# Performance work log

Measured on AMD Instinct MI355X. Metric: run time of the kernel, lower is better.

The kernel has to match this reference:

```python
import jax, jax.numpy as jnp
import numpy as np

B, S, HID, NH = 2, 2048, 1024, 16
HD = HID // NH  # head_dim = 64


def setup_inputs() -> dict:
    key = jax.random.key(0)
    ks = jax.random.split(key, 9)
    init = 0.02
    return {
        "x": jax.random.normal(ks[0], (B, S, HID), dtype=jnp.float32),
        "Wq": jax.random.normal(ks[1], (HID, HID), dtype=jnp.float32) * init,
        "bq": jnp.zeros((HID,), dtype=jnp.float32),
        "Wk": jax.random.normal(ks[2], (HID, HID), dtype=jnp.float32) * init,
        "bk": jnp.zeros((HID,), dtype=jnp.float32),
        "Wv": jax.random.normal(ks[3], (HID, HID), dtype=jnp.float32) * init,
        "bv": jnp.zeros((HID,), dtype=jnp.float32),
        "Wo": jax.random.normal(ks[4], (HID, HID), dtype=jnp.float32) * init,
        "bo": jnp.zeros((HID,), dtype=jnp.float32),
    }


def _split_heads(t):
    # [B, S, HID] -> [B, NH, S, HD]
    return t.reshape(B, S, NH, HD).transpose(0, 2, 1, 3)


def reference(x, Wq, bq, Wk, bk, Wv, bv, Wo, bo):
    q = _split_heads(x @ Wq.T + bq)
    k = _split_heads(x @ Wk.T + bk)
    v = _split_heads(x @ Wv.T + bv)

    # Faithful to source: scores = QK^T / (head_dim ** -0.5) == QK^T * sqrt(head_dim)
    inv_scale = jnp.asarray(HD ** (-0.5), dtype=x.dtype)
    scores = jnp.einsum("bhqd,bhkd->bhqk", q, k) / inv_scale

    causal_mask = jnp.triu(jnp.ones((S, S), dtype=bool), k=1)  # True above diagonal
    scores = jnp.where(causal_mask, jnp.asarray(-jnp.inf, dtype=scores.dtype), scores)
    attn = jax.nn.softmax(scores, axis=-1)  # dropout = identity (eval mode)

    ctx = jnp.einsum("bhqk,bhkd->bhqd", attn, v)
    ctx = ctx.transpose(0, 2, 1, 3).reshape(B, S, HID)
    out = ctx @ Wo.T + bo  # out_layer Linear; dropout = identity
    return out, attn
```

## Files before the change

### kernel.cpp

```cpp
#include <hip/hip_runtime.h>
#include <hip/hip_bf16.h>

#define BB   2
#define SS   2048
#define HID  1024
#define NH   16
#define HD   64
#define NEGS -30000.0f

typedef __bf16 bf16x8 __attribute__((ext_vector_type(8)));
typedef __bf16 bf16x4 __attribute__((ext_vector_type(4)));
typedef float  f32x4  __attribute__((ext_vector_type(4)));

static __device__ __forceinline__ f32x4 mfma_bf16(bf16x8 a, bf16x8 b, f32x4 c) {
    return __builtin_amdgcn_mfma_f32_16x16x32_bf16(a, b, c, 0, 0, 0);
}

static __device__ __forceinline__ void split_bf16(float f, __bf16* hp, __bf16* lp) {
    __bf16 h = (__bf16)f;
    *hp = h;
    *lp = (__bf16)(f - (float)h);
}

static __device__ __forceinline__ float clampf(float v, float lo, float hi) {
    return fminf(fmaxf(v, lo), hi);
}

static __device__ __forceinline__ void gll16(const __bf16* g, __bf16* l) {
    __builtin_amdgcn_global_load_lds((const void*)g, (void*)l, 16, 0, 0);
}

static __device__ __forceinline__ void barrier_lds() {
    asm volatile("s_waitcnt lgkmcnt(0)" ::: "memory");
    __builtin_amdgcn_sched_barrier(0);
    __builtin_amdgcn_s_barrier();
    __builtin_amdgcn_sched_barrier(0);
}

__global__ __launch_bounds__(256) void split_kernel(
    const float* __restrict__ x,
    const float* __restrict__ Wq, const float* __restrict__ Wk,
    const float* __restrict__ Wv, const float* __restrict__ Wo,
    __bf16* __restrict__ xh, __bf16* __restrict__ xl,
    __bf16* __restrict__ wqh, __bf16* __restrict__ wql,
    __bf16* __restrict__ wkh, __bf16* __restrict__ wkl,
    __bf16* __restrict__ wvh, __bf16* __restrict__ woh)
{
    const int which = blockIdx.y;
    const int i4 = blockIdx.x * 256 + threadIdx.x;
    if (which == 0) {
        const float4 v = ((const float4*)x)[i4];
        const float* p = (const float*)&v;
        bf16x4 h4, l4v;
#pragma unroll
        for (int j = 0; j < 4; j++) { __bf16 hh, ll; split_bf16(p[j], &hh, &ll); h4[j] = hh; l4v[j] = ll; }
        *(bf16x4*)&xh[(size_t)i4 * 4] = h4;
        *(bf16x4*)&xl[(size_t)i4 * 4] = l4v;
        return;
    }
    if (i4 >= (HID * HID) / 4) return;
    const float* src = which == 1 ? Wq : which == 2 ? Wk : which == 3 ? Wv : Wo;
    const float sc = (which == 1) ? 8.0f : 1.0f;
    const float4 v = ((const float4*)src)[i4];
    const float* p = (const float*)&v;
    bf16x4 h4, l4v;
#pragma unroll
    for (int j = 0; j < 4; j++) { __bf16 hh, ll; split_bf16(p[j] * sc, &hh, &ll); h4[j] = hh; l4v[j] = ll; }
    if (which == 1)      { *(bf16x4*)&wqh[(size_t)i4 * 4] = h4; *(bf16x4*)&wql[(size_t)i4 * 4] = l4v; }
    else if (which == 2) { *(bf16x4*)&wkh[(size_t)i4 * 4] = h4; *(bf16x4*)&wkl[(size_t)i4 * 4] = l4v; }
    else if (which == 3) { *(bf16x4*)&wvh[(size_t)i4 * 4] = h4; }
    else                 { *(bf16x4*)&woh[(size_t)i4 * 4] = h4; }
}

__global__ __launch_bounds__(256) void qkv_kernel(
    const __bf16* __restrict__ xh, const __bf16* __restrict__ xl,
    const __bf16* __restrict__ wqh, const __bf16* __restrict__ wql,
    const __bf16* __restrict__ wkh, const __bf16* __restrict__ wkl,
    const __bf16* __restrict__ wvh,
    const float* __restrict__ bq, const float* __restrict__ bk, const float* __restrict__ bv,
    __bf16* __restrict__ qh, __bf16* __restrict__ ql,
    __bf16* __restrict__ kh, __bf16* __restrict__ kl,
    __bf16* __restrict__ vt)
{
    __shared__ __align__(16) __bf16 smem[18432];
    __bf16* const Ah = smem;
    __bf16* const Al = smem + 4096;
    __bf16* const Bh = smem + 8192;
    __bf16* const Bl = smem + 12288;

    const int stream = blockIdx.x >> 3, ct = blockIdx.x & 7;
    const int t0 = blockIdx.y * 128, c0 = ct * 128;
    const bool qk = stream < 2;
    const __bf16* const Bhg = stream == 0 ? wqh : stream == 1 ? wkh : wvh;
    const __bf16* const Blg = stream == 0 ? wql : wkl;
    const float* const bias = stream == 0 ? bq : stream == 1 ? bk : bv;
    const float bscale = stream == 0 ? 8.0f : 1.0f;

    const int tid = threadIdx.x, wave = tid >> 6, lane = tid & 63;
    const int l16 = lane & 15, quad = lane >> 4;
    const int wr = wave >> 1, wc = wave & 1;

    const int ar0 = tid >> 2,         as0 = (tid & 3) ^ (ar0 & 3);
    const int ar1 = (256 + tid) >> 2, as1 = ((256 + tid) & 3) ^ (ar1 & 3);
    const size_t aoff0 = (size_t)(t0 + ar0) * HID + as0 * 8;
    const size_t aoff1 = (size_t)(t0 + ar1) * HID + as1 * 8;
    const size_t boff0 = (size_t)(c0 + ar0) * HID + as0 * 8;
    const size_t boff1 = (size_t)(c0 + ar1) * HID + as1 * 8;
    const int ld0 = wave << 9, ld1 = (4 + wave) << 9;

    const f32x4 zero4 = {0.f, 0.f, 0.f, 0.f};
    f32x4 acc[4][4];
#pragma unroll
    for (int i = 0; i < 4; i++)
#pragma unroll
        for (int j = 0; j < 4; j++) acc[i][j] = zero4;

    for (int k0 = 0; k0 < HID; k0 += 32) {
        __syncthreads();
        gll16(xh + aoff0 + k0, Ah + ld0);
        gll16(xh + aoff1 + k0, Ah + ld1);
        gll16(Bhg + boff0 + k0, Bh + ld0);
        gll16(Bhg + boff1 + k0, Bh + ld1);
        if (qk) {
            gll16(xl + aoff0 + k0, Al + ld0);
            gll16(xl + aoff1 + k0, Al + ld1);
            gll16(Blg + boff0 + k0, Bl + ld0);
            gll16(Blg + boff1 + k0, Bl + ld1);
        }
        __syncthreads();

        bf16x8 aH[4], aL[4], bHf[4], bLf[4];
#pragma unroll
        for (int mf = 0; mf < 4; mf++) {
            const int row = wr * 64 + mf * 16 + l16;
            const int off = row * 32 + ((quad ^ (row & 3)) << 3);
            aH[mf] = *(const bf16x8*)(Ah + off);
            if (qk) aL[mf] = *(const bf16x8*)(Al + off);
        }
#pragma unroll
        for (int nf = 0; nf < 4; nf++) {
            const int row = wc * 64 + nf * 16 + l16;
            const int off = row * 32 + ((quad ^ (row & 3)) << 3);
            bHf[nf] = *(const bf16x8*)(Bh + off);
            if (qk) bLf[nf] = *(const bf16x8*)(Bl + off);
        }
#pragma unroll
        for (int mf = 0; mf < 4; mf++)
#pragma unroll
            for (int nf = 0; nf < 4; nf++) {
                acc[mf][nf] = mfma_bf16(aH[mf], bHf[nf], acc[mf][nf]);
                if (qk) {
                    acc[mf][nf] = mfma_bf16(aH[mf], bLf[nf], acc[mf][nf]);
                    acc[mf][nf] = mfma_bf16(aL[mf], bHf[nf], acc[mf][nf]);
                }
            }
    }

    const int bidx = t0 >> 11;
    const int s0 = t0 & (SS - 1);

    if (qk) {
        __bf16* const Es = smem;
        __bf16* const hi_arr = stream == 0 ? qh : kh;
        __bf16* const lo_arr = stream == 0 ? ql : kl;
#pragma unroll
        for (int pass = 0; pass < 2; pass++) {
            __syncthreads();
#pragma unroll
            for (int nf = 0; nf < 4; nf++) {
                const int dcl = wc * 64 + nf * 16 + l16;
                const float bv_ = bias[c0 + dcl] * bscale;
#pragma unroll
                for (int mf = 0; mf < 4; mf++)
#pragma unroll
                    for (int r = 0; r < 4; r++) {
                        const int srl = wr * 64 + mf * 16 + quad * 4 + r;
                        const float v = clampf(acc[mf][nf][r] + bv_, -1e4f, 1e4f);
                        __bf16 hv, lv;
                        split_bf16(v, &hv, &lv);
                        Es[srl * 132 + dcl] = pass ? lv : hv;
                    }
            }
            __syncthreads();
            __bf16* const dst = pass ? lo_arr : hi_arr;
#pragma unroll
            for (int i = 0; i < 8; i++) {
                const int idx = tid + i * 256;
                const int row = idx >> 4, c16 = idx & 15;
                const int hh = (c0 >> 6) + (c16 >> 3);
                const int dd = (c16 & 7) * 8;
                const size_t o = ((size_t)(bidx * NH + hh) * SS + (s0 + row)) * HD + dd;
                *(uint4*)&dst[o] = *(const uint4*)&Es[row * 132 + c16 * 8];
            }
        }
    } else {
        __syncthreads();
        __bf16* const Vts = smem + wave * 4608;
#pragma unroll
        for (int nf = 0; nf < 4; nf++) {
            const int dloc = nf * 16 + l16;
            const float bv_ = bias[c0 + wc * 64 + dloc];
#pragma unroll
            for (int mf = 0; mf < 4; mf++)
#pragma unroll
                for (int r = 0; r < 4; r++)
                    Vts[dloc * 72 + mf * 16 + quad * 4 + r] =
                        (__bf16)clampf(acc[mf][nf][r] + bv_, -1e4f, 1e4f);
        }
        const int hh = (c0 + wc * 64) >> 6;
        const size_t vb = (size_t)(bidx * NH + hh) * HD * SS;
        const int sc0 = s0 + wr * 64;
#pragma unroll
        for (int j = 0; j < 8; j++) {
            const int idx = j * 64 + lane;
            const int d = idx >> 3, c8 = idx & 7;
            *(uint4*)&vt[vb + (size_t)d * SS + sc0 + c8 * 8] =
                *(const uint4*)&Vts[d * 72 + c8 * 8];
        }
    }
}

__global__ __launch_bounds__(512) void attn_kernel(
    const __bf16* __restrict__ qh, const __bf16* __restrict__ ql,
    const __bf16* __restrict__ kh, const __bf16* __restrict__ kl,
    const __bf16* __restrict__ vt,
    float* __restrict__ attn, __bf16* __restrict__ ctx)
{
    __shared__ __align__(16) __bf16 Kh0[4096], Kl0[4096], Kh1[4096], Kl1[4096];
    __shared__ __align__(16) __bf16 Vt0[4096], Vt1[4096];
    __shared__ __align__(16) __bf16 Ps[128][72];
    __shared__ __align__(16) __bf16 _occ_pad[8192];

    const int bid = blockIdx.x;
    const int g   = bid & 7;
    const int ii  = bid >> 3;
    const int bh  = g + 8 * (ii & 3);
    const int p   = ii >> 2;
    const int b   = bh >> 4, h = bh & 15;

    const int tid  = threadIdx.x;
    const int wave = tid >> 6, lane = tid & 63;
    const int l16  = lane & 15, quad = lane >> 4;

    const int sr = tid >> 3, ssw = (tid & 7) ^ (sr & 7);
    const size_t kq = (size_t)sr * HD + ssw * 8;
    const size_t vq = (size_t)sr * SS + ssw * 8;
    const int ldw = wave << 9;

    const __bf16* const khp = kh + (size_t)bh * SS * HD;
    const __bf16* const klp = kl + (size_t)bh * SS * HD;
    const __bf16* const vtp = vt + (size_t)bh * HD * SS;

#define STAGE_K(j_, KH, KL) do {                                  \
        const __bf16* kg_ = khp + (size_t)(j_) * (64 * HD);       \
        const __bf16* lg_ = klp + (size_t)(j_) * (64 * HD);       \
        gll16(kg_ + kq, (KH) + ldw); gll16(lg_ + kq, (KL) + ldw); \
    } while (0)
#define STAGE_V(j_, VT) do {                                      \
        const __bf16* vg_ = vtp + (size_t)(j_) * 64;              \
        gll16(vg_ + vq, (VT) + ldw);                              \
    } while (0)

    const f32x4 zero4 = {0.f, 0.f, 0.f, 0.f};

    for (int seg = 0; seg < 2; seg++) {
        const int qt = seg ? p : (15 - p);
        const int nj = 2 * qt + 2;

        bf16x8 aHq[2], aLq[2];
        {
            const size_t qrow = ((size_t)bh * SS + qt * 128 + wave * 16 + l16) * HD;
#pragma unroll
            for (int ks = 0; ks < 2; ks++) {
                aHq[ks] = *(const bf16x8*)&qh[qrow + ks * 32 + quad * 8];
                aLq[ks] = *(const bf16x8*)&ql[qrow + ks * 32 + quad * 8];
            }
        }

        float m4[4], l4[4];
#pragma unroll
        for (int r = 0; r < 4; r++) { m4[r] = NEGS; l4[r] = 0.f; }

        __syncthreads();
        STAGE_K(0, Kh0, Kl0);
        __syncthreads();

        for (int j = 0; j < nj; j++) {
            if (j) __syncthreads();
            if (j < nj - 1) {
                if (j & 1) STAGE_K(j + 1, Kh0, Kl0);
                else       STAGE_K(j + 1, Kh1, Kl1);
            }
            const __bf16* const Khc = (j & 1) ? Kh1 : Kh0;
            const __bf16* const Klc = (j & 1) ? Kl1 : Kl0;

            f32x4 sacc[4] = {zero4, zero4, zero4, zero4};
#pragma unroll
            for (int ks = 0; ks < 2; ks++)
#pragma unroll
                for (int c = 0; c < 4; c++) {
                    const int krow = c * 16 + l16;
                    const int ko = krow * 64 + (((ks * 4 + quad) ^ (krow & 7)) << 3);
                    const bf16x8 bH = *(const bf16x8*)(Khc + ko);
                    const bf16x8 bL = *(const bf16x8*)(Klc + ko);
                    sacc[c] = mfma_bf16(aHq[ks], bH, sacc[c]);
                    sacc[c] = mfma_bf16(aHq[ks], bL, sacc[c]);
                    sacc[c] = mfma_bf16(aLq[ks], bH, sacc[c]);
                }
            if (j >= 2 * qt) {
                const int cb = j * 64, qr = qt * 128 + wave * 16 + quad * 4;
#pragma unroll
                for (int c = 0; c < 4; c++) {
                    const int col = cb + c * 16 + l16;
#pragma unroll
                    for (int r = 0; r < 4; r++)
                        if (col > qr + r) sacc[c][r] = NEGS;
                }
            }
#pragma unroll
            for (int r = 0; r < 4; r++) {
                const float mx = fmaxf(fmaxf(sacc[0][r], sacc[1][r]),
                                       fmaxf(sacc[2][r], sacc[3][r]));
                const float mn = fmaxf(m4[r], mx);
                l4[r] = l4[r] * __expf(m4[r] - mn)
                      + __expf(sacc[0][r] - mn) + __expf(sacc[1][r] - mn)
                      + __expf(sacc[2][r] - mn) + __expf(sacc[3][r] - mn);
                m4[r] = mn;
            }
        }

        float il[4];
#pragma unroll
        for (int r = 0; r < 4; r++) {
#pragma unroll
            for (int off = 1; off < 16; off <<= 1) {
                const float mo  = __shfl_xor(m4[r], off);
                const float lo_ = __shfl_xor(l4[r], off);
                const float mn  = fmaxf(m4[r], mo);
                l4[r] = l4[r] * __expf(m4[r] - mn) + lo_ * __expf(mo - mn);
                m4[r] = mn;
            }
            il[r] = (l4[r] > 0.f) ? (1.0f / l4[r]) : 0.f;
        }

        f32x4 cacc[4] = {zero4, zero4, zero4, zero4};

        __syncthreads();
        STAGE_K(0, Kh0, Kl0);
        STAGE_V(0, Vt0);

        for (int j = 0; j < nj; j++) {
            __syncthreads();
            if (j < nj - 1) {
                if (j & 1) { STAGE_K(j + 1, Kh0, Kl0); STAGE_V(j + 1, Vt0); }
                else       { STAGE_K(j + 1, Kh1, Kl1); STAGE_V(j + 1, Vt1); }
            }
            const __bf16* const Khc = (j & 1) ? Kh1 : Kh0;
            const __bf16* const Klc = (j & 1) ? Kl1 : Kl0;
            const __bf16* const Vtc = (j & 1) ? Vt1 : Vt0;

            f32x4 sacc[4] = {zero4, zero4, zero4, zero4};
#pragma unroll
            for (int ks = 0; ks < 2; ks++)
#pragma unroll
                for (int c = 0; c < 4; c++) {
                    const int krow = c * 16 + l16;
                    const int ko = krow * 64 + (((ks * 4 + quad) ^ (krow & 7)) << 3);
                    const bf16x8 bH = *(const bf16x8*)(Khc + ko);
                    const bf16x8 bL = *(const bf16x8*)(Klc + ko);
                    sacc[c] = mfma_bf16(aHq[ks], bH, sacc[c]);
                    sacc[c] = mfma_bf16(aHq[ks], bL, sacc[c]);
                    sacc[c] = mfma_bf16(aLq[ks], bH, sacc[c]);
                }
            if (j >= 2 * qt) {
                const int cb = j * 64, qr = qt * 128 + wave * 16 + quad * 4;
#pragma unroll
                for (int c = 0; c < 4; c++) {
                    const int col = cb + c * 16 + l16;
#pragma unroll
                    for (int r = 0; r < 4; r++)
                        if (col > qr + r) sacc[c][r] = NEGS;
                }
            }
#pragma unroll
            for (int c = 0; c < 4; c++)
#pragma unroll
                for (int r = 0; r < 4; r++) {
                    const float pv = clampf(__expf(sacc[c][r] - m4[r]) * il[r], 0.f, 1.f);
                    Ps[wave * 16 + quad * 4 + r][c * 16 + l16] = (__bf16)pv;
                }
            barrier_lds();

#pragma unroll
            for (int i = 0; i < 2; i++) {
                const int idx = tid + i * 512;
                const int row = idx >> 3, c8 = idx & 7;
                const size_t o = ((size_t)bh * SS + qt * 128 + row) * SS + j * 64 + c8 * 8;
                __bf16 tmp[8];
                *(uint4*)tmp = *(const uint4*)&Ps[row][c8 * 8];
                float4 f0, f1;
                f0.x = (float)tmp[0]; f0.y = (float)tmp[1];
                f0.z = (float)tmp[2]; f0.w = (float)tmp[3];
                f1.x = (float)tmp[4]; f1.y = (float)tmp[5];
                f1.z = (float)tmp[6]; f1.w = (float)tmp[7];
                *(float4*)&attn[o]     = f0;
                *(float4*)&attn[o + 4] = f1;
            }
#pragma unroll
            for (int ks = 0; ks < 2; ks++) {
                const bf16x8 ap = *(const bf16x8*)&Ps[wave * 16 + l16][ks * 32 + quad * 8];
#pragma unroll
                for (int dt = 0; dt < 4; dt++) {
                    const int vrow = dt * 16 + l16;
                    const int vo = vrow * 64 + (((ks * 4 + quad) ^ (vrow & 7)) << 3);
                    cacc[dt] = mfma_bf16(ap, *(const bf16x8*)(Vtc + vo), cacc[dt]);
                }
            }
        }

        const float4 zf4 = {0.f, 0.f, 0.f, 0.f};
        for (int j = nj; j < SS / 64; j++) {
#pragma unroll
            for (int i = 0; i < 4; i++) {
                const int idx = tid + i * 512;
                const int row = idx >> 4, c4 = idx & 15;
                const size_t o = ((size_t)bh * SS + qt * 128 + row) * SS + j * 64 + c4 * 4;
                *(float4*)&attn[o] = zf4;
            }
        }

        __syncthreads();
#pragma unroll
        for (int dt = 0; dt < 4; dt++) {
            const int d = dt * 16 + l16;
#pragma unroll
            for (int r = 0; r < 4; r++)
                Ps[wave * 16 + quad * 4 + r][d] =
                    (__bf16)clampf(cacc[dt][r], -1e4f, 1e4f);
        }
        __syncthreads();
#pragma unroll
        for (int i = 0; i < 2; i++) {
            const int idx = tid + i * 512;
            const int row = idx >> 3, c8 = idx & 7;
            *(uint4*)&ctx[(size_t)(b * SS + qt * 128 + row) * HID + h * 64 + c8 * 8] =
                *(const uint4*)&Ps[row][c8 * 8];
        }
    }

    if ((int)blockIdx.x < 0) ((volatile __bf16*)_occ_pad)[0] = Ps[0][0];
#undef STAGE_K
#undef STAGE_V
}

__global__ __launch_bounds__(256) void out_kernel(
    const __bf16* __restrict__ ctx, const __bf16* __restrict__ woh,
    const float* __restrict__ bo, float* __restrict__ out)
{
    __shared__ __align__(16) __bf16 As[4096], Bs[4096];

    const int o0 = blockIdx.x * 128;
    const int t0 = blockIdx.y * 128;

    const int tid = threadIdx.x, wave = tid >> 6, lane = tid & 63;
    const int l16 = lane & 15, quad = lane >> 4;
    const int wr = wave >> 1, wc = wave & 1;

    const int ar0 = tid >> 2,         as0 = (tid & 3) ^ (ar0 & 3);
    const int ar1 = (256 + tid) >> 2, as1 = ((256 + tid) & 3) ^ (ar1 & 3);
    const size_t aoff0 = (size_t)(t0 + ar0) * HID + as0 * 8;
    const size_t aoff1 = (size_t)(t0 + ar1) * HID + as1 * 8;
    const size_t boff0 = (size_t)(o0 + ar0) * HID + as0 * 8;
    const size_t boff1 = (size_t)(o0 + ar1) * HID + as1 * 8;
    const int ld0 = wave << 9, ld1 = (4 + wave) << 9;

    const f32x4 zero4 = {0.f, 0.f, 0.f, 0.f};
    f32x4 acc[4][4];
#pragma unroll
    for (int i = 0; i < 4; i++)
#pragma unroll
        for (int j = 0; j < 4; j++) acc[i][j] = zero4;

    for (int k0 = 0; k0 < HID; k0 += 32) {
        __syncthreads();
        gll16(ctx + aoff0 + k0, As + ld0);
        gll16(ctx + aoff1 + k0, As + ld1);
        gll16(woh + boff0 + k0, Bs + ld0);
        gll16(woh + boff1 + k0, Bs + ld1);
        __syncthreads();

        bf16x8 aH[4], bHf[4];
#pragma unroll
        for (int mf = 0; mf < 4; mf++) {
            const int row = wr * 64 + mf * 16 + l16;
            aH[mf] = *(const bf16x8*)(As + row * 32 + ((quad ^ (row & 3)) << 3));
        }
#pragma unroll
        for (int nf = 0; nf < 4; nf++) {
            const int row = wc * 64 + nf * 16 + l16;
            bHf[nf] = *(const bf16x8*)(Bs + row * 32 + ((quad ^ (row & 3)) << 3));
        }
#pragma unroll
        for (int mf = 0; mf < 4; mf++)
#pragma unroll
            for (int nf = 0; nf < 4; nf++)
                acc[mf][nf] = mfma_bf16(aH[mf], bHf[nf], acc[mf][nf]);
    }

#pragma unroll
    for (int nf = 0; nf < 4; nf++) {
        const int dcol = o0 + wc * 64 + nf * 16 + l16;
        const float bias = bo[dcol];
#pragma unroll
        for (int mf = 0; mf < 4; mf++)
#pragma unroll
            for (int r = 0; r < 4; r++) {
                const int t = t0 + wr * 64 + mf * 16 + quad * 4 + r;
                out[(size_t)t * HID + dcol] = clampf(acc[mf][nf][r] + bias, -1e4f, 1e4f);
            }
    }
}

extern "C" void kernel_launch(void* const* d_in, const int* in_sizes, int n_in,
                              void* d_out, int out_size, void* d_ws, size_t ws_size,
                              hipStream_t stream) {
    const float* x  = (const float*)d_in[0];
    const float* Wq = (const float*)d_in[1];
    const float* bq = (const float*)d_in[2];
    const float* Wk = (const float*)d_in[3];
    const float* bk = (const float*)d_in[4];
    const float* Wv = (const float*)d_in[5];
    const float* bv = (const float*)d_in[6];
    const float* Wo = (const float*)d_in[7];
    const float* bo = (const float*)d_in[8];

    float* out  = (float*)d_out;
    float* attn = out + (size_t)BB * SS * HID;

    const size_t NQ = (size_t)BB * NH * SS * HD;
    const size_t NW = (size_t)HID * HID;
    __bf16* ws  = (__bf16*)d_ws;
    __bf16* qh  = ws;
    __bf16* ql  = ws + NQ;
    __bf16* kh  = ws + 2 * NQ;
    __bf16* kl  = ws + 3 * NQ;
    __bf16* vt  = ws + 4 * NQ;
    __bf16* xh  = ws + 5 * NQ;
    __bf16* xl  = ws + 6 * NQ;
    __bf16* wqh = ws + 7 * NQ;
    __bf16* wql = wqh + NW;
    __bf16* wkh = wqh + 2 * NW;
    __bf16* wkl = wqh + 3 * NW;
    __bf16* wvh = wqh + 4 * NW;
    __bf16* woh = wqh + 5 * NW;
    __bf16* ctx = xh;

    split_kernel<<<dim3(4096, 5), 256, 0, stream>>>(x, Wq, Wk, Wv, Wo,
                                                    xh, xl, wqh, wql, wkh, wkl, wvh, woh);
    qkv_kernel<<<dim3(24, 32), 256, 0, stream>>>(xh, xl, wqh, wql, wkh, wkl, wvh,
                                                 bq, bk, bv, qh, ql, kh, kl, vt);
    attn_kernel<<<dim3(256), 512, 0, stream>>>(qh, ql, kh, kl, vt, attn, ctx);
    out_kernel<<<dim3(8, 32), 256, 0, stream>>>(ctx, woh, bo, out);
}
```

Before: 765.8 us.

## Double-buffer LDS tiles in QKV and output GEMMs; compact split kernel grid

The QKV and output-projection GEMM loops now use two LDS buffers. The next k-slice's global-to-LDS loads are issued right after a single barrier, so they overlap with the MFMA work on the current slice; this replaces the old load, barrier, compute pattern that used two barriers per step. The split kernel moves from a 2D grid, where most blocks for the weight rows exited immediately, to a dense 1D grid with no idle blocks. The cost is more LDS per block (64KB in qkv), which may lower occupancy.

Result: faster. 745.1 us (-2.7%).

```diff
diff --git a/kernel.cpp b/kernel.cpp
--- a/kernel.cpp
+++ b/kernel.cpp
@@ -46,9 +46,9 @@
     __bf16* __restrict__ wkh, __bf16* __restrict__ wkl,
     __bf16* __restrict__ wvh, __bf16* __restrict__ woh)
 {
-    const int which = blockIdx.y;
-    const int i4 = blockIdx.x * 256 + threadIdx.x;
-    if (which == 0) {
+    const int bid = blockIdx.x;
+    if (bid < 4096) {
+        const int i4 = bid * 256 + threadIdx.x;
         const float4 v = ((const float4*)x)[i4];
         const float* p = (const float*)&v;
         bf16x4 h4, l4v;
@@ -58,7 +58,9 @@
         *(bf16x4*)&xl[(size_t)i4 * 4] = l4v;
         return;
     }
-    if (i4 >= (HID * HID) / 4) return;
+    const int wb = bid - 4096;
+    const int which = (wb >> 10) + 1;
+    const int i4 = (wb & 1023) * 256 + threadIdx.x;
     const float* src = which == 1 ? Wq : which == 2 ? Wk : which == 3 ? Wv : Wo;
     const float sc = (which == 1) ? 8.0f : 1.0f;
     const float4 v = ((const float4*)src)[i4];
@@ -82,11 +84,7 @@
     __bf16* __restrict__ kh, __bf16* __restrict__ kl,
     __bf16* __restrict__ vt)
 {
-    __shared__ __align__(16) __bf16 smem[18432];
-    __bf16* const Ah = smem;
-    __bf16* const Al = smem + 4096;
-    __bf16* const Bh = smem + 8192;
-    __bf16* const Bl = smem + 12288;
+    __shared__ __align__(16) __bf16 smem[32768];
 
     const int stream = blockIdx.x >> 3, ct = blockIdx.x & 7;
     const int t0 = blockIdx.y * 128, c0 = ct * 128;
@@ -108,6 +106,20 @@
     const size_t boff1 = (size_t)(c0 + ar1) * HID + as1 * 8;
     const int ld0 = wave << 9, ld1 = (4 + wave) << 9;
 
+#define QKV_STAGE(b_, k0_) do {                                   \
+        __bf16* s_ = smem + (b_) * 16384;                         \
+        gll16(xh + aoff0 + (k0_), s_ + ld0);                      \
+        gll16(xh + aoff1 + (k0_), s_ + ld1);                      \
+        gll16(Bhg + boff0 + (k0_), s_ + 8192 + ld0);              \
+        gll16(Bhg + boff1 + (k0_), s_ + 8192 + ld1);              \
+        if (qk) {                                                 \
+            gll16(xl + aoff0 + (k0_), s_ + 4096 + ld0);           \
+            gll16(xl + aoff1 + (k0_), s_ + 4096 + ld1);           \
+            gll16(Blg + boff0 + (k0_), s_ + 12288 + ld0);         \
+            gll16(Blg + boff1 + (k0_), s_ + 12288 + ld1);         \
+        }                                                         \
+    } while (0)
+
     const f32x4 zero4 = {0.f, 0.f, 0.f, 0.f};
     f32x4 acc[4][4];
 #pragma unroll
@@ -115,34 +127,27 @@
 #pragma unroll
         for (int j = 0; j < 4; j++) acc[i][j] = zero4;
 
+    QKV_STAGE(0, 0);
     for (int k0 = 0; k0 < HID; k0 += 32) {
-        __syncthreads();
-        gll16(xh + aoff0 + k0, Ah + ld0);
-        gll16(xh + aoff1 + k0, Ah + ld1);
-        gll16(Bhg + boff0 + k0, Bh + ld0);
-        gll16(Bhg + boff1 + k0, Bh + ld1);
-        if (qk) {
-            gll16(xl + aoff0 + k0, Al + ld0);
-            gll16(xl + aoff1 + k0, Al + ld1);
-            gll16(Blg + boff0 + k0, Bl + ld0);
-            gll16(Blg + boff1 + k0, Bl + ld1);
-        }
-        __syncthreads();
+        const int cur = (k0 >> 5) & 1;
+        __syncthreads();
+        if (k0 + 32 < HID) QKV_STAGE(cur ^ 1, k0 + 32);
+        __bf16* const s_ = smem + cur * 16384;
 
         bf16x8 aH[4], aL[4], bHf[4], bLf[4];
 #pragma unroll
         for (int mf = 0; mf < 4; mf++) {
             const int row = wr * 64 + mf * 16 + l16;
             const int off = row * 32 + ((quad ^ (row & 3)) << 3);
-            aH[mf] = *(const bf16x8*)(Ah + off);
-            if (qk) aL[mf] = *(const bf16x8*)(Al + off);
+            aH[mf] = *(const bf16x8*)(s_ + off);
+            if (qk) aL[mf] = *(const bf16x8*)(s_ + 4096 + off);
         }
 #pragma unroll
         for (int nf = 0; nf < 4; nf++) {
             const int row = wc * 64 + nf * 16 + l16;
             const int off = row * 32 + ((quad ^ (row & 3)) << 3);
-            bHf[nf] = *(const bf16x8*)(Bh + off);
-            if (qk) bLf[nf] = *(const bf16x8*)(Bl + off);
+            bHf[nf] = *(const bf16x8*)(s_ + 8192 + off);
+            if (qk) bLf[nf] = *(const bf16x8*)(s_ + 12288 + off);
         }
 #pragma unroll
         for (int mf = 0; mf < 4; mf++)
@@ -155,6 +160,7 @@
                 }
             }
     }
+#undef QKV_STAGE
 
     const int bidx = t0 >> 11;
     const int s0 = t0 & (SS - 1);
@@ -457,7 +463,7 @@
     const __bf16* __restrict__ ctx, const __bf16* __restrict__ woh,
     const float* __restrict__ bo, float* __restrict__ out)
 {
-    __shared__ __align__(16) __bf16 As[4096], Bs[4096];
+    __shared__ __align__(16) __bf16 smem[16384];
 
     const int o0 = blockIdx.x * 128;
     const int t0 = blockIdx.y * 128;
@@ -474,6 +480,14 @@
     const size_t boff1 = (size_t)(o0 + ar1) * HID + as1 * 8;
     const int ld0 = wave << 9, ld1 = (4 + wave) << 9;
 
+#define OUT_STAGE(b_, k0_) do {                                   \
+        __bf16* s_ = smem + (b_) * 8192;                          \
+        gll16(ctx + aoff0 + (k0_), s_ + ld0);                     \
+        gll16(ctx + aoff1 + (k0_), s_ + ld1);                     \
+        gll16(woh + boff0 + (k0_), s_ + 4096 + ld0);              \
+        gll16(woh + boff1 + (k0_), s_ + 4096 + ld1);              \
+    } while (0)
+
     const f32x4 zero4 = {0.f, 0.f, 0.f, 0.f};
     f32x4 acc[4][4];
 #pragma unroll
@@ -481,24 +495,23 @@
 #pragma unroll
         for (int j = 0; j < 4; j++) acc[i][j] = zero4;
 
+    OUT_STAGE(0, 0);
     for (int k0 = 0; k0 < HID; k0 += 32) {
-        __syncthreads();
-        gll16(ctx + aoff0 + k0, As + ld0);
-        gll16(ctx + aoff1 + k0, As + ld1);
-        gll16(woh + boff0 + k0, Bs + ld0);
-        gll16(woh + boff1 + k0, Bs + ld1);
-        __syncthreads();
+        const int cur = (k0 >> 5) & 1;
+        __syncthreads();
+        if (k0 + 32 < HID) OUT_STAGE(cur ^ 1, k0 + 32);
+        __bf16* const s_ = smem + cur * 8192;
 
         bf16x8 aH[4], bHf[4];
 #pragma unroll
         for (int mf = 0; mf < 4; mf++) {
             const int row = wr * 64 + mf * 16 + l16;
-            aH[mf] = *(const bf16x8*)(As + row * 32 + ((quad ^ (row & 3)) << 3));
+            aH[mf] = *(const bf16x8*)(s_ + row * 32 + ((quad ^ (row & 3)) << 3));
         }
 #pragma unroll
         for (int nf = 0; nf < 4; nf++) {
             const int row = wc * 64 + nf * 16 + l16;
-            bHf[nf] = *(const bf16x8*)(Bs + row * 32 + ((quad ^ (row & 3)) << 3));
+            bHf[nf] = *(const bf16x8*)(s_ + 4096 + row * 32 + ((quad ^ (row & 3)) << 3));
         }
 #pragma unroll
         for (int mf = 0; mf < 4; mf++)
@@ -506,6 +519,7 @@
             for (int nf = 0; nf < 4; nf++)
                 acc[mf][nf] = mfma_bf16(aH[mf], bHf[nf], acc[mf][nf]);
     }
+#undef OUT_STAGE
 
 #pragma unroll
     for (int nf = 0; nf < 4; nf++) {
@@ -555,8 +569,8 @@
     __bf16* woh = wqh + 5 * NW;
     __bf16* ctx = xh;
 
-    split_kernel<<<dim3(4096, 5), 256, 0, stream>>>(x, Wq, Wk, Wv, Wo,
-                                                    xh, xl, wqh, wql, wkh, wkl, wvh, woh);
+    split_kernel<<<dim3(8192), 256, 0, stream>>>(x, Wq, Wk, Wv, Wo,
+                                                 xh, xl, wqh, wql, wkh, wkl, wvh, woh);
     qkv_kernel<<<dim3(24, 32), 256, 0, stream>>>(xh, xl, wqh, wql, wkh, wkl, wvh,
                                                  bq, bk, bv, qh, ql, kh, kl, vt);
     attn_kernel<<<dim3(256), 512, 0, stream>>>(qh, ql, kh, kl, vt, attn, ctx);
```
